# Performance work log

Measured on AMD Instinct MI355X. Metric: run time of the kernel, lower is better.

The kernel has to match this reference:

```python
import jax, jax.numpy as jnp
import numpy as np

B, T, DIM = 64, 1, 2048
HQ, HK, D = 16, 4, 128
S_PAST = 4095
EPS = 1e-5
MIN_TS, MAX_TS = 1.0, 10000.0


def setup_inputs() -> dict:
    key = jax.random.key(0)
    ks = jax.random.split(key, 8)
    return {
        "x": jax.random.normal(ks[0], (B, T, DIM), dtype=jnp.float32),
        "pos": jax.random.randint(ks[1], (B, T), 0, S_PAST, dtype=jnp.int64),
        "k_cache": jax.random.normal(ks[2], (B, HK, S_PAST, D), dtype=jnp.float32),
        "v_cache": jax.random.normal(ks[3], (B, HK, S_PAST, D), dtype=jnp.float32),
        "Wq": jax.random.normal(ks[4], (HQ * D, DIM), dtype=jnp.float32) * 0.02,
        "Wk": jax.random.normal(ks[5], (HK * D, DIM), dtype=jnp.float32) * 0.02,
        "Wv": jax.random.normal(ks[6], (HK * D, DIM), dtype=jnp.float32) * 0.02,
        "Wo": jax.random.normal(ks[7], (DIM, HQ * D), dtype=jnp.float32) * 0.02,
        "qn_w": jnp.ones((D,), dtype=jnp.float32),
        "kn_w": jnp.ones((D,), dtype=jnp.float32),
    }


def _rmsnorm(t, w):
    return t * jax.lax.rsqrt(jnp.mean(t * t, axis=-1, keepdims=True) + EPS) * w


def reference(x, pos, k_cache, v_cache, Wq, Wk, Wv, Wo, qn_w, kn_w):
    # projections (fp32), reshape to heads: [B, T, H, D]
    q = (x @ Wq.T).reshape(B, T, HQ, D)
    k = (x @ Wk.T).reshape(B, T, HK, D)
    v = (x @ Wv.T).reshape(B, T, HK, D)

    q = _rmsnorm(q, qn_w)
    k = _rmsnorm(k, kn_w)

    # RoPE: emb built from pos [B, T] -> [B, T, 1, D] broadcast over heads
    half = D // 2
    fraction = 2.0 * jnp.arange(half, dtype=jnp.float32) / D
    inv_freq = 1.0 / (MIN_TS * (MAX_TS / MIN_TS) ** fraction)
    freqs = pos.astype(jnp.float32)[..., None] * inv_freq          # [B, T, half]
    emb = jnp.concatenate([freqs, freqs], axis=-1)[:, :, None, :]   # [B, T, 1, D]
    cos, sin = jnp.cos(emb), jnp.sin(emb)

    def rope(t):
        t1, t2 = jnp.split(t, 2, axis=-1)
        return t * cos + jnp.concatenate([-t2, t1], axis=-1) * sin

    q = rope(q)
    k = rope(k)

    # [B, H, T, D]
    q = q.transpose(0, 2, 1, 3)
    k = k.transpose(0, 2, 1, 3)
    v = v.transpose(0, 2, 1, 3)

    # KV-cache append -> full kv length S_PAST + 1
    kf = jnp.concatenate([k_cache, k], axis=2)  # [B, HK, S+1, D]
    vf = jnp.concatenate([v_cache, v], axis=2)

    # GQA SDPA with scale=1.0 (explicit in the torch module)
    G = HQ // HK
    qg = q.reshape(B, HK, G * T, D)             # group queries under kv heads
    scores = jnp.einsum("bhqd,bhkd->bhqk", qg, kf)
    probs = jax.nn.softmax(scores, axis=-1)
    attn = jnp.einsum("bhqk,bhkd->bhqd", probs, vf)  # [B, HK, G*T, D]
    attn = attn.reshape(B, HQ, T, D).transpose(0, 2, 1, 3).reshape(B, T, HQ * D)

    return attn @ Wo.T  # [B, T, DIM]
```

## Files before the change

### kernel.cpp

```cpp
#include <hip/hip_runtime.h>
#include <math.h>

#define DIM    2048
#define B_     64
#define HQ     16
#define HK     4
#define G_     4
#define D_     128
#define SPAST  4095
#define SEQ    4096
#define NSPLIT 8
#define KSPLIT 8
#define EPS    1e-5f

typedef short bfrag __attribute__((ext_vector_type(8)));
typedef float facc  __attribute__((ext_vector_type(4)));
typedef unsigned short ushort_t;

__device__ inline unsigned short f2bf(float f) {
    unsigned u = __float_as_uint(f);
    return (unsigned short)((u + 0x7FFFu + ((u >> 16) & 1u)) >> 16);
}

template<bool ABF16>
__global__ __launch_bounds__(256) void gemm_mfma_kernel(
    const void* __restrict__ Aptr,
    const float* __restrict__ W0, const float* __restrict__ W1,
    const float* __restrict__ W2,
    float* __restrict__ part, int N)
{
    const int K  = 2048;
    const int KS = K / KSPLIT;
    int n0 = blockIdx.x * 64;
    int ks = blockIdx.y;
    const float* W; int wc;
    if (n0 < 2048)      { W = W0; wc = n0; }
    else if (n0 < 2560) { W = W1; wc = n0 - 2048; }
    else                { W = W2; wc = n0 - 2560; }

    __shared__ bfrag a_lds[64 * 8];
    __shared__ bfrag w_lds[64 * 8];

    int t = threadIdx.x;
    int w = t >> 6, l = t & 63;
    int row_s = t >> 2;
    int q_s   = t & 3;
    int sw_s  = row_s & 7;
    int c0    = q_s * 2;

    facc acc[4] = {};

    const float*    Af = (const float*)Aptr;
    const ushort_t* Ab = (const ushort_t*)Aptr;
    size_t a_off = (size_t)row_s * K + (size_t)ks * KS + q_s * 16;
    const float* Wbase = W + (size_t)(wc + row_s) * K + (size_t)ks * KS + q_s * 16;

    for (int kt = 0; kt < KS; kt += 64) {
        __syncthreads();
        if constexpr (ABF16) {
            const ushort_t* p = Ab + a_off + kt;
            bfrag v0 = *(const bfrag*)(p);
            bfrag v1 = *(const bfrag*)(p + 8);
            a_lds[row_s * 8 + ((c0    ) ^ sw_s)] = v0;
            a_lds[row_s * 8 + ((c0 + 1) ^ sw_s)] = v1;
        } else {
            const float* p = Af + a_off + kt;
            float4 f0 = *(const float4*)(p);
            float4 f1 = *(const float4*)(p + 4);
            float4 f2 = *(const float4*)(p + 8);
            float4 f3 = *(const float4*)(p + 12);
            bfrag v0, v1;
            v0[0]=f2bf(f0.x); v0[1]=f2bf(f0.y); v0[2]=f2bf(f0.z); v0[3]=f2bf(f0.w);
            v0[4]=f2bf(f1.x); v0[5]=f2bf(f1.y); v0[6]=f2bf(f1.z); v0[7]=f2bf(f1.w);
            v1[0]=f2bf(f2.x); v1[1]=f2bf(f2.y); v1[2]=f2bf(f2.z); v1[3]=f2bf(f2.w);
            v1[4]=f2bf(f3.x); v1[5]=f2bf(f3.y); v1[6]=f2bf(f3.z); v1[7]=f2bf(f3.w);
            a_lds[row_s * 8 + ((c0    ) ^ sw_s)] = v0;
            a_lds[row_s * 8 + ((c0 + 1) ^ sw_s)] = v1;
        }
        {
            const float* p = Wbase + kt;
            float4 f0 = *(const float4*)(p);
            float4 f1 = *(const float4*)(p + 4);
            float4 f2 = *(const float4*)(p + 8);
            float4 f3 = *(const float4*)(p + 12);
            bfrag v0, v1;
            v0[0]=f2bf(f0.x); v0[1]=f2bf(f0.y); v0[2]=f2bf(f0.z); v0[3]=f2bf(f0.w);
            v0[4]=f2bf(f1.x); v0[5]=f2bf(f1.y); v0[6]=f2bf(f1.z); v0[7]=f2bf(f1.w);
            v1[0]=f2bf(f2.x); v1[1]=f2bf(f2.y); v1[2]=f2bf(f2.z); v1[3]=f2bf(f2.w);
            v1[4]=f2bf(f3.x); v1[5]=f2bf(f3.y); v1[6]=f2bf(f3.z); v1[7]=f2bf(f3.w);
            w_lds[row_s * 8 + ((c0    ) ^ sw_s)] = v0;
            w_lds[row_s * 8 + ((c0 + 1) ^ sw_s)] = v1;
        }
        __syncthreads();
        #pragma unroll
        for (int kc = 0; kc < 2; ++kc) {
            int nrow = w * 16 + (l & 15);
            bfrag bf = w_lds[nrow * 8 + ((kc * 4 + (l >> 4)) ^ (nrow & 7))];
            #pragma unroll
            for (int rg = 0; rg < 4; ++rg) {
                int arow = rg * 16 + (l & 15);
                bfrag af = a_lds[arow * 8 + ((kc * 4 + (l >> 4)) ^ (arow & 7))];
                acc[rg] = __builtin_amdgcn_mfma_f32_16x16x32_bf16(af, bf, acc[rg], 0, 0, 0);
            }
        }
    }
    #pragma unroll
    for (int rg = 0; rg < 4; ++rg) {
        #pragma unroll
        for (int r = 0; r < 4; ++r) {
            int row = rg * 16 + (l >> 4) * 4 + r;
            int col = n0 + w * 16 + (l & 15);
            part[((size_t)ks * 64 + row) * N + col] = acc[rg][r];
        }
    }
}

__global__ __launch_bounds__(256) void rope_norm_kernel(
    const float* __restrict__ part1, const int* __restrict__ pos,
    const float* __restrict__ qn_w, const float* __restrict__ kn_w,
    float* __restrict__ qr, float* __restrict__ kr, float* __restrict__ vr)
{
    int row  = blockIdx.x * 4 + (threadIdx.x >> 6);
    int lane = threadIdx.x & 63;
    int b = row / 24, h = row % 24;
    int col, type;
    if (h < 16)      { type = 0; col = h * 128; }
    else if (h < 20) { type = 1; col = 2048 + (h - 16) * 128; }
    else             { type = 2; col = 2560 + (h - 20) * 128; }

    float t1 = 0.f, t2 = 0.f;
    #pragma unroll
    for (int ksp = 0; ksp < KSPLIT; ++ksp) {
        t1 += part1[((size_t)ksp * 64 + b) * 3072 + col + lane];
        t2 += part1[((size_t)ksp * 64 + b) * 3072 + col + lane + 64];
    }

    if (type == 2) {
        vr[(b * HK + (h - 20)) * 128 + lane]      = t1;
        vr[(b * HK + (h - 20)) * 128 + lane + 64] = t2;
        return;
    }

    float ss = t1 * t1 + t2 * t2;
    ss += __shfl_xor(ss, 1);  ss += __shfl_xor(ss, 2);  ss += __shfl_xor(ss, 4);
    ss += __shfl_xor(ss, 8);  ss += __shfl_xor(ss, 16); ss += __shfl_xor(ss, 32);
    float rn = 1.0f / sqrtf(ss * (1.0f / 128.0f) + EPS);
    const float* wn = (type == 0) ? qn_w : kn_w;
    float n1 = t1 * rn * wn[lane];
    float n2 = t2 * rn * wn[lane + 64];

    float invf = powf(10000.0f, -(float)lane * (1.0f / 64.0f));
    float f    = (float)pos[b] * invf;
    float sv = sinf(f), cv = cosf(f);
    float o1 = n1 * cv - n2 * sv;
    float o2 = n2 * cv + n1 * sv;

    if (type == 0) {
        qr[(b * HQ + h) * 128 + lane]      = o1;
        qr[(b * HQ + h) * 128 + lane + 64] = o2;
    } else {
        kr[(b * HK + (h - 16)) * 128 + lane]      = o1;
        kr[(b * HK + (h - 16)) * 128 + lane + 64] = o2;
    }
}

__global__ __launch_bounds__(256) void attn_kernel(
    const float* __restrict__ kc, const float* __restrict__ vc,
    const float* __restrict__ qr, const float* __restrict__ kr,
    const float* __restrict__ vr,
    float* __restrict__ pacc, float* __restrict__ pml)
{
    int blk  = blockIdx.x;
    int sp   = blk & (NSPLIT - 1);
    int hk   = (blk >> 3) & (HK - 1);
    int b    = blk >> 5;
    int t    = threadIdx.x;
    int wh   = t >> 5;
    int l32  = t & 31;
    int g    = t & 3;
    int dbase = (l32 >> 2) * 16;
    int sel1 = l32 & 1, sel2 = l32 & 2;

    float4 q4[G_];
    #pragma unroll
    for (int gg = 0; gg < G_; ++gg)
        q4[gg] = *(const float4*)&qr[(size_t)(b * HQ + hk * G_ + gg) * D_ + l32 * 4];

    const float* kbase = kc + (size_t)(b * HK + hk) * SPAST * D_;
    const float* vbase = vc + (size_t)(b * HK + hk) * SPAST * D_;
    const float* knew  = kr + (b * HK + hk) * D_;
    const float* vnew  = vr + (b * HK + hk) * D_;

    float  m = -1e30f, lsum = 0.f;
    float4 acc[4];
    #pragma unroll
    for (int j = 0; j < 4; ++j) acc[j] = make_float4(0.f, 0.f, 0.f, 0.f);

    auto COMPUTE = [&](const float4& k4, const float4* v4) {
        float p0 = q4[0].x*k4.x + q4[0].y*k4.y + q4[0].z*k4.z + q4[0].w*k4.w;
        float p1 = q4[1].x*k4.x + q4[1].y*k4.y + q4[1].z*k4.z + q4[1].w*k4.w;
        float p2 = q4[2].x*k4.x + q4[2].y*k4.y + q4[2].z*k4.z + q4[2].w*k4.w;
        float p3 = q4[3].x*k4.x + q4[3].y*k4.y + q4[3].z*k4.z + q4[3].w*k4.w;
        float ka = sel1 ? p1 : p0, sa = sel1 ? p0 : p1;
        float kb = sel1 ? p3 : p2, sb = sel1 ? p2 : p3;
        float s01 = ka + __shfl_xor(sa, 1);
        float s23 = kb + __shfl_xor(sb, 1);
        float kc2 = sel2 ? s23 : s01, sc = sel2 ? s01 : s23;
        float p = kc2 + __shfl_xor(sc, 2);
        p += __shfl_xor(p, 4);
        p += __shfl_xor(p, 8);
        p += __shfl_xor(p, 16);
        if (p > m + 8.0f) {
            float al = __expf(m - p);
            m = p;
            lsum *= al;
            #pragma unroll
            for (int j = 0; j < 4; ++j) {
                acc[j].x *= al; acc[j].y *= al; acc[j].z *= al; acc[j].w *= al;
            }
        }
        float e = __expf(p - m);
        lsum += e;
        #pragma unroll
        for (int j = 0; j < 4; ++j) {
            acc[j].x += e * v4[j].x; acc[j].y += e * v4[j].y;
            acc[j].z += e * v4[j].z; acc[j].w += e * v4[j].w;
        }
    };

    int off = (sp * 512 + wh) * D_;
    float4 k4 = *(const float4*)(kbase + off + l32 * 4);
    float4 v4[4];
    #pragma unroll
    for (int j = 0; j < 4; ++j)
        v4[j] = *(const float4*)(vbase + off + dbase + j * 4);

    for (int i = 0; i < 62; ++i) {
        int offn = off + 8 * D_;
        float4 k4n = *(const float4*)(kbase + offn + l32 * 4);
        float4 v4n[4];
        #pragma unroll
        for (int j = 0; j < 4; ++j)
            v4n[j] = *(const float4*)(vbase + offn + dbase + j * 4);
        COMPUTE(k4, v4);
        k4 = k4n;
        #pragma unroll
        for (int j = 0; j < 4; ++j) v4[j] = v4n[j];
        off = offn;
    }
    COMPUTE(k4, v4);
    {
        int s_f = sp * 512 + 504 + wh;
        const float* kp = (s_f < SPAST) ? (kbase + (size_t)s_f * D_ + l32 * 4)
                                        : (knew + l32 * 4);
        const float* vp = (s_f < SPAST) ? (vbase + (size_t)s_f * D_ + dbase)
                                        : (vnew + dbase);
        k4 = *(const float4*)kp;
        #pragma unroll
        for (int j = 0; j < 4; ++j) v4[j] = *(const float4*)(vp + j * 4);
        COMPUTE(k4, v4);
    }

    __shared__ float s_acc[8][G_][D_];
    __shared__ float s_m[8][G_];
    __shared__ float s_l[8][G_];
    #pragma unroll
    for (int j = 0; j < 4; ++j)
        *(float4*)&s_acc[wh][g][dbase + j * 4] = acc[j];
    if (l32 < 4) { s_m[wh][l32] = m; s_l[wh][l32] = lsum; }
    __syncthreads();

    if (t < 128) {
        int d = t;
        #pragma unroll
        for (int gg = 0; gg < G_; ++gg) {
            float M = -1e30f;
            #pragma unroll
            for (int j = 0; j < 8; ++j) M = fmaxf(M, s_m[j][gg]);
            float L = 0.f, a = 0.f;
            #pragma unroll
            for (int j = 0; j < 8; ++j) {
                float e = __expf(s_m[j][gg] - M);
                L += e * s_l[j][gg];
                a += e * s_acc[j][gg][d];
            }
            int hq = hk * G_ + gg;
            size_t pidx = (size_t)(b * HQ + hq) * NSPLIT + sp;
            pacc[pidx * D_ + d] = a;
            if (d == 0) { pml[pidx * 2 + 0] = M; pml[pidx * 2 + 1] = L; }
        }
    }
}

__global__ void attn_combine_kernel(const float* __restrict__ pacc,
                                    const float* __restrict__ pml,
                                    ushort_t* __restrict__ attnb)
{
    int bh = blockIdx.x;
    int d  = threadIdx.x;
    float M = -1e30f;
    #pragma unroll
    for (int s = 0; s < NSPLIT; ++s)
        M = fmaxf(M, pml[(size_t)(bh * NSPLIT + s) * 2]);
    float L = 0.f, a = 0.f;
    #pragma unroll
    for (int s = 0; s < NSPLIT; ++s) {
        float e = __expf(pml[(size_t)(bh * NSPLIT + s) * 2] - M);
        L += e * pml[(size_t)(bh * NSPLIT + s) * 2 + 1];
        a += e * pacc[(size_t)(bh * NSPLIT + s) * D_ + d];
    }
    attnb[(size_t)bh * D_ + d] = f2bf(a / L);
}

__global__ void sum_parts_kernel(const float* __restrict__ part,
                                 float* __restrict__ out)
{
    int i = blockIdx.x * 256 + threadIdx.x;
    float v = 0.f;
    #pragma unroll
    for (int ksp = 0; ksp < KSPLIT; ++ksp)
        v += part[(size_t)ksp * B_ * DIM + i];
    out[i] = v;
}

extern "C" void kernel_launch(void* const* d_in, const int* in_sizes, int n_in,
                              void* d_out, int out_size, void* d_ws, size_t ws_size,
                              hipStream_t stream)
{
    const float* x   = (const float*)d_in[0];
    const int*   pos = (const int*)  d_in[1];
    const float* kc  = (const float*)d_in[2];
    const float* vc  = (const float*)d_in[3];
    const float* Wq  = (const float*)d_in[4];
    const float* Wk  = (const float*)d_in[5];
    const float* Wv  = (const float*)d_in[6];
    const float* Wo  = (const float*)d_in[7];
    const float* qn  = (const float*)d_in[8];
    const float* kn  = (const float*)d_in[9];

    float* ws    = (float*)d_ws;
    float* part1 = ws;
    float* qr    = part1 + (size_t)KSPLIT * 64 * 3072;
    float* kr    = qr    + (size_t)64 * HQ * D_;
    float* vr    = kr    + (size_t)64 * HK * D_;
    float* pacc  = vr    + (size_t)64 * HK * D_;
    float* pml   = pacc  + (size_t)64 * HQ * NSPLIT * D_;
    float* attnb = pml   + (size_t)64 * HQ * NSPLIT * 2;
    float* part4 = attnb + (size_t)64 * DIM;

    gemm_mfma_kernel<false><<<dim3(48, KSPLIT), 256, 0, stream>>>(
        x, Wq, Wk, Wv, part1, 3072);
    rope_norm_kernel<<<384, 256, 0, stream>>>(part1, pos, qn, kn, qr, kr, vr);
    attn_kernel<<<B_ * HK * NSPLIT, 256, 0, stream>>>(kc, vc, qr, kr, vr, pacc, pml);
    attn_combine_kernel<<<B_ * HQ, 128, 0, stream>>>(pacc, pml, (ushort_t*)attnb);
    gemm_mfma_kernel<true><<<dim3(32, KSPLIT), 256, 0, stream>>>(
        attnb, Wo, Wo, Wo, part4, 2048);
    sum_parts_kernel<<<(B_ * DIM) / 256, 256, 0, stream>>>(part4, (float*)d_out);
}
```

Measured before the change: 224.0 us.

## Double GEMM K-split and issue all tile loads upfront in projection kernel

Raises the split-K factor from 8 to 16, doubling the number of GEMM blocks. Each block now covers exactly two 64-wide K tiles, so the tile loop is replaced by straight-line code. Global loads for both tiles are issued before any conversion or MFMA work, so memory latency overlaps with compute. The cost is twice as many partial-sum rows to write and reduce, plus higher register pressure from holding both tiles' data at once.

```diff
diff --git a/kernel.cpp b/kernel.cpp
--- a/kernel.cpp
+++ b/kernel.cpp
@@ -10,7 +10,7 @@
 #define SPAST  4095
 #define SEQ    4096
 #define NSPLIT 8
-#define KSPLIT 8
+#define KSPLIT 16
 #define EPS    1e-5f
 
 typedef short bfrag __attribute__((ext_vector_type(8)));
@@ -20,6 +20,13 @@
 __device__ inline unsigned short f2bf(float f) {
     unsigned u = __float_as_uint(f);
     return (unsigned short)((u + 0x7FFFu + ((u >> 16) & 1u)) >> 16);
+}
+
+__device__ inline bfrag pack8(const float4& f0, const float4& f1) {
+    bfrag v;
+    v[0]=f2bf(f0.x); v[1]=f2bf(f0.y); v[2]=f2bf(f0.z); v[3]=f2bf(f0.w);
+    v[4]=f2bf(f1.x); v[5]=f2bf(f1.y); v[6]=f2bf(f1.z); v[7]=f2bf(f1.w);
+    return v;
 }
 
 template<bool ABF16>
@@ -55,43 +62,32 @@
     size_t a_off = (size_t)row_s * K + (size_t)ks * KS + q_s * 16;
     const float* Wbase = W + (size_t)(wc + row_s) * K + (size_t)ks * KS + q_s * 16;
 
-    for (int kt = 0; kt < KS; kt += 64) {
-        __syncthreads();
-        if constexpr (ABF16) {
-            const ushort_t* p = Ab + a_off + kt;
-            bfrag v0 = *(const bfrag*)(p);
-            bfrag v1 = *(const bfrag*)(p + 8);
-            a_lds[row_s * 8 + ((c0    ) ^ sw_s)] = v0;
-            a_lds[row_s * 8 + ((c0 + 1) ^ sw_s)] = v1;
-        } else {
-            const float* p = Af + a_off + kt;
-            float4 f0 = *(const float4*)(p);
-            float4 f1 = *(const float4*)(p + 4);
-            float4 f2 = *(const float4*)(p + 8);
-            float4 f3 = *(const float4*)(p + 12);
-            bfrag v0, v1;
-            v0[0]=f2bf(f0.x); v0[1]=f2bf(f0.y); v0[2]=f2bf(f0.z); v0[3]=f2bf(f0.w);
-            v0[4]=f2bf(f1.x); v0[5]=f2bf(f1.y); v0[6]=f2bf(f1.z); v0[7]=f2bf(f1.w);
-            v1[0]=f2bf(f2.x); v1[1]=f2bf(f2.y); v1[2]=f2bf(f2.z); v1[3]=f2bf(f2.w);
-            v1[4]=f2bf(f3.x); v1[5]=f2bf(f3.y); v1[6]=f2bf(f3.z); v1[7]=f2bf(f3.w);
-            a_lds[row_s * 8 + ((c0    ) ^ sw_s)] = v0;
-            a_lds[row_s * 8 + ((c0 + 1) ^ sw_s)] = v1;
-        }
-        {
-            const float* p = Wbase + kt;
-            float4 f0 = *(const float4*)(p);
-            float4 f1 = *(const float4*)(p + 4);
-            float4 f2 = *(const float4*)(p + 8);
-            float4 f3 = *(const float4*)(p + 12);
-            bfrag v0, v1;
-            v0[0]=f2bf(f0.x); v0[1]=f2bf(f0.y); v0[2]=f2bf(f0.z); v0[3]=f2bf(f0.w);
-            v0[4]=f2bf(f1.x); v0[5]=f2bf(f1.y); v0[6]=f2bf(f1.z); v0[7]=f2bf(f1.w);
-            v1[0]=f2bf(f2.x); v1[1]=f2bf(f2.y); v1[2]=f2bf(f2.z); v1[3]=f2bf(f2.w);
-            v1[4]=f2bf(f3.x); v1[5]=f2bf(f3.y); v1[6]=f2bf(f3.z); v1[7]=f2bf(f3.w);
-            w_lds[row_s * 8 + ((c0    ) ^ sw_s)] = v0;
-            w_lds[row_s * 8 + ((c0 + 1) ^ sw_s)] = v1;
-        }
-        __syncthreads();
+    bfrag a0b0, a0b1, a1b0, a1b1;
+    float4 a0f0, a0f1, a0f2, a0f3;
+    float4 a1f0, a1f1, a1f2, a1f3;
+    if constexpr (ABF16) {
+        const ushort_t* p0 = Ab + a_off;
+        a0b0 = *(const bfrag*)(p0);  a0b1 = *(const bfrag*)(p0 + 8);
+        const ushort_t* p1 = Ab + a_off + 64;
+        a1b0 = *(const bfrag*)(p1);  a1b1 = *(const bfrag*)(p1 + 8);
+    } else {
+        const float* p0 = Af + a_off;
+        a0f0 = *(const float4*)(p0);     a0f1 = *(const float4*)(p0 + 4);
+        a0f2 = *(const float4*)(p0 + 8); a0f3 = *(const float4*)(p0 + 12);
+        const float* p1 = Af + a_off + 64;
+        a1f0 = *(const float4*)(p1);     a1f1 = *(const float4*)(p1 + 4);
+        a1f2 = *(const float4*)(p1 + 8); a1f3 = *(const float4*)(p1 + 12);
+    }
+    float4 w0f0 = *(const float4*)(Wbase);
+    float4 w0f1 = *(const float4*)(Wbase + 4);
+    float4 w0f2 = *(const float4*)(Wbase + 8);
+    float4 w0f3 = *(const float4*)(Wbase + 12);
+    float4 w1f0 = *(const float4*)(Wbase + 64);
+    float4 w1f1 = *(const float4*)(Wbase + 68);
+    float4 w1f2 = *(const float4*)(Wbase + 72);
+    float4 w1f3 = *(const float4*)(Wbase + 76);
+
+    auto mfma_step = [&]() {
         #pragma unroll
         for (int kc = 0; kc < 2; ++kc) {
             int nrow = w * 16 + (l & 15);
@@ -103,7 +99,32 @@
                 acc[rg] = __builtin_amdgcn_mfma_f32_16x16x32_bf16(af, bf, acc[rg], 0, 0, 0);
             }
         }
-    }
+    };
+
+    if constexpr (ABF16) {
+        a_lds[row_s * 8 + ((c0    ) ^ sw_s)] = a0b0;
+        a_lds[row_s * 8 + ((c0 + 1) ^ sw_s)] = a0b1;
+    } else {
+        a_lds[row_s * 8 + ((c0    ) ^ sw_s)] = pack8(a0f0, a0f1);
+        a_lds[row_s * 8 + ((c0 + 1) ^ sw_s)] = pack8(a0f2, a0f3);
+    }
+    w_lds[row_s * 8 + ((c0    ) ^ sw_s)] = pack8(w0f0, w0f1);
+    w_lds[row_s * 8 + ((c0 + 1) ^ sw_s)] = pack8(w0f2, w0f3);
+    __syncthreads();
+    mfma_step();
+    __syncthreads();
+    if constexpr (ABF16) {
+        a_lds[row_s * 8 + ((c0    ) ^ sw_s)] = a1b0;
+        a_lds[row_s * 8 + ((c0 + 1) ^ sw_s)] = a1b1;
+    } else {
+        a_lds[row_s * 8 + ((c0    ) ^ sw_s)] = pack8(a1f0, a1f1);
+        a_lds[row_s * 8 + ((c0 + 1) ^ sw_s)] = pack8(a1f2, a1f3);
+    }
+    w_lds[row_s * 8 + ((c0    ) ^ sw_s)] = pack8(w1f0, w1f1);
+    w_lds[row_s * 8 + ((c0 + 1) ^ sw_s)] = pack8(w1f2, w1f3);
+    __syncthreads();
+    mfma_step();
+
     #pragma unroll
     for (int rg = 0; rg < 4; ++rg) {
         #pragma unroll
```

After: 226.1 us. About the same (+0.9%).

## Map one KV row per 64-lane wavefront in attention to cut registers

Applied to the files above, without the earlier changes.

Restructures the split-KV attention kernel so each 64-lane wavefront handles one key/value row per step instead of each 32-lane half handling one. Each lane now holds two K elements and eight V elements, which halves the per-thread accumulator and prefetch registers, and the launch bounds request higher occupancy. In exchange the 4-wave block walks 4 rows per step over 128 iterations, each score needs an extra cross-lane shuffle, and fewer rows are in flight per wave.

```diff
diff --git a/kernel.cpp b/kernel.cpp
--- a/kernel.cpp
+++ b/kernel.cpp
@@ -164,7 +164,7 @@
     }
 }
 
-__global__ __launch_bounds__(256) void attn_kernel(
+__global__ __launch_bounds__(256, 8) void attn_kernel(
     const float* __restrict__ kc, const float* __restrict__ vc,
     const float* __restrict__ qr, const float* __restrict__ kr,
     const float* __restrict__ vr,
@@ -175,16 +175,16 @@
     int hk   = (blk >> 3) & (HK - 1);
     int b    = blk >> 5;
     int t    = threadIdx.x;
-    int wh   = t >> 5;
-    int l32  = t & 31;
-    int g    = t & 3;
-    int dbase = (l32 >> 2) * 16;
-    int sel1 = l32 & 1, sel2 = l32 & 2;
-
-    float4 q4[G_];
+    int w    = t >> 6;
+    int l    = t & 63;
+    int g    = l & 3;
+    int dbase = (l >> 2) * 8;
+    int sel1 = l & 1, sel2 = l & 2;
+
+    float2 q2[G_];
     #pragma unroll
     for (int gg = 0; gg < G_; ++gg)
-        q4[gg] = *(const float4*)&qr[(size_t)(b * HQ + hk * G_ + gg) * D_ + l32 * 4];
+        q2[gg] = *(const float2*)&qr[(size_t)(b * HQ + hk * G_ + gg) * D_ + l * 2];
 
     const float* kbase = kc + (size_t)(b * HK + hk) * SPAST * D_;
     const float* vbase = vc + (size_t)(b * HK + hk) * SPAST * D_;
@@ -192,15 +192,14 @@
     const float* vnew  = vr + (b * HK + hk) * D_;
 
     float  m = -1e30f, lsum = 0.f;
-    float4 acc[4];
-    #pragma unroll
-    for (int j = 0; j < 4; ++j) acc[j] = make_float4(0.f, 0.f, 0.f, 0.f);
-
-    auto COMPUTE = [&](const float4& k4, const float4* v4) {
-        float p0 = q4[0].x*k4.x + q4[0].y*k4.y + q4[0].z*k4.z + q4[0].w*k4.w;
-        float p1 = q4[1].x*k4.x + q4[1].y*k4.y + q4[1].z*k4.z + q4[1].w*k4.w;
-        float p2 = q4[2].x*k4.x + q4[2].y*k4.y + q4[2].z*k4.z + q4[2].w*k4.w;
-        float p3 = q4[3].x*k4.x + q4[3].y*k4.y + q4[3].z*k4.z + q4[3].w*k4.w;
+    float4 acc0 = make_float4(0.f, 0.f, 0.f, 0.f);
+    float4 acc1 = make_float4(0.f, 0.f, 0.f, 0.f);
+
+    auto COMPUTE = [&](const float2& k2, const float4& v0, const float4& v1) {
+        float p0 = q2[0].x * k2.x + q2[0].y * k2.y;
+        float p1 = q2[1].x * k2.x + q2[1].y * k2.y;
+        float p2 = q2[2].x * k2.x + q2[2].y * k2.y;
+        float p3 = q2[3].x * k2.x + q2[3].y * k2.y;
         float ka = sel1 ? p1 : p0, sa = sel1 ? p0 : p1;
         float kb = sel1 ? p3 : p2, sb = sel1 ? p2 : p3;
         float s01 = ka + __shfl_xor(sa, 1);
@@ -210,64 +209,54 @@
         p += __shfl_xor(p, 4);
         p += __shfl_xor(p, 8);
         p += __shfl_xor(p, 16);
+        p += __shfl_xor(p, 32);
         if (p > m + 8.0f) {
             float al = __expf(m - p);
             m = p;
             lsum *= al;
-            #pragma unroll
-            for (int j = 0; j < 4; ++j) {
-                acc[j].x *= al; acc[j].y *= al; acc[j].z *= al; acc[j].w *= al;
-            }
+            acc0.x *= al; acc0.y *= al; acc0.z *= al; acc0.w *= al;
+            acc1.x *= al; acc1.y *= al; acc1.z *= al; acc1.w *= al;
         }
         float e = __expf(p - m);
         lsum += e;
-        #pragma unroll
-        for (int j = 0; j < 4; ++j) {
-            acc[j].x += e * v4[j].x; acc[j].y += e * v4[j].y;
-            acc[j].z += e * v4[j].z; acc[j].w += e * v4[j].w;
-        }
+        acc0.x += e * v0.x; acc0.y += e * v0.y;
+        acc0.z += e * v0.z; acc0.w += e * v0.w;
+        acc1.x += e * v1.x; acc1.y += e * v1.y;
+        acc1.z += e * v1.z; acc1.w += e * v1.w;
     };
 
-    int off = (sp * 512 + wh) * D_;
-    float4 k4 = *(const float4*)(kbase + off + l32 * 4);
-    float4 v4[4];
-    #pragma unroll
-    for (int j = 0; j < 4; ++j)
-        v4[j] = *(const float4*)(vbase + off + dbase + j * 4);
-
-    for (int i = 0; i < 62; ++i) {
-        int offn = off + 8 * D_;
-        float4 k4n = *(const float4*)(kbase + offn + l32 * 4);
-        float4 v4n[4];
-        #pragma unroll
-        for (int j = 0; j < 4; ++j)
-            v4n[j] = *(const float4*)(vbase + offn + dbase + j * 4);
-        COMPUTE(k4, v4);
-        k4 = k4n;
-        #pragma unroll
-        for (int j = 0; j < 4; ++j) v4[j] = v4n[j];
-        off = offn;
-    }
-    COMPUTE(k4, v4);
+    int off = (sp * 512 + w) * D_;
+    float2 k2 = *(const float2*)(kbase + off + l * 2);
+    float4 v0 = *(const float4*)(vbase + off + dbase);
+    float4 v1 = *(const float4*)(vbase + off + dbase + 4);
+
+    for (int i = 0; i < 126; ++i) {
+        int offn = off + 4 * D_;
+        float2 k2n = *(const float2*)(kbase + offn + l * 2);
+        float4 v0n = *(const float4*)(vbase + offn + dbase);
+        float4 v1n = *(const float4*)(vbase + offn + dbase + 4);
+        COMPUTE(k2, v0, v1);
+        k2 = k2n; v0 = v0n; v1 = v1n; off = offn;
+    }
+    COMPUTE(k2, v0, v1);
     {
-        int s_f = sp * 512 + 504 + wh;
-        const float* kp = (s_f < SPAST) ? (kbase + (size_t)s_f * D_ + l32 * 4)
-                                        : (knew + l32 * 4);
+        int s_f = sp * 512 + 508 + w;
+        const float* kp = (s_f < SPAST) ? (kbase + (size_t)s_f * D_ + l * 2)
+                                        : (knew + l * 2);
         const float* vp = (s_f < SPAST) ? (vbase + (size_t)s_f * D_ + dbase)
                                         : (vnew + dbase);
-        k4 = *(const float4*)kp;
-        #pragma unroll
-        for (int j = 0; j < 4; ++j) v4[j] = *(const float4*)(vp + j * 4);
-        COMPUTE(k4, v4);
-    }
-
-    __shared__ float s_acc[8][G_][D_];
-    __shared__ float s_m[8][G_];
-    __shared__ float s_l[8][G_];
-    #pragma unroll
-    for (int j = 0; j < 4; ++j)
-        *(float4*)&s_acc[wh][g][dbase + j * 4] = acc[j];
-    if (l32 < 4) { s_m[wh][l32] = m; s_l[wh][l32] = lsum; }
+        k2 = *(const float2*)kp;
+        v0 = *(const float4*)(vp);
+        v1 = *(const float4*)(vp + 4);
+        COMPUTE(k2, v0, v1);
+    }
+
+    __shared__ float s_acc[4][G_][D_];
+    __shared__ float s_m[4][G_];
+    __shared__ float s_l[4][G_];
+    *(float4*)&s_acc[w][g][dbase]     = acc0;
+    *(float4*)&s_acc[w][g][dbase + 4] = acc1;
+    if (l < 4) { s_m[w][l] = m; s_l[w][l] = lsum; }
     __syncthreads();
 
     if (t < 128) {
@@ -276,10 +265,10 @@
         for (int gg = 0; gg < G_; ++gg) {
             float M = -1e30f;
             #pragma unroll
-            for (int j = 0; j < 8; ++j) M = fmaxf(M, s_m[j][gg]);
+            for (int j = 0; j < 4; ++j) M = fmaxf(M, s_m[j][gg]);
             float L = 0.f, a = 0.f;
             #pragma unroll
-            for (int j = 0; j < 8; ++j) {
+            for (int j = 0; j < 4; ++j) {
                 float e = __expf(s_m[j][gg] - M);
                 L += e * s_l[j][gg];
                 a += e * s_acc[j][gg][d];
```

Measured after the change: 258.7 us. 15.5% more time.
